# Performance work log

Hardware: AMD Instinct MI355X
Metric: run time of the kernel (lower is better)

## Reference

```python
import jax, jax.numpy as jnp
import numpy as np
from jax.scipy.special import logsumexp

B, T, D, H, K = 32, 512, 768, 256, 32


def setup_inputs() -> dict:
    key = jax.random.key(0)
    ks = jax.random.split(key, 12)
    x = jax.random.normal(ks[0], (B, T, D), jnp.float32)
    lengths = jax.random.randint(ks[1], (B,), T // 2, T + 1).astype(jnp.int32)
    mask = jnp.arange(T)[None, :] < lengths[:, None]  # [B,T] bool
    targets = jax.random.randint(ks[2], (B, T), 0, K)

    def p(k, shape, fan):
        return jax.random.normal(k, shape, jnp.float32) / np.sqrt(fan).astype(np.float32)

    W_ih_f = p(ks[3], (4 * H, D), D); W_hh_f = p(ks[4], (4 * H, H), H)
    W_ih_b = p(ks[5], (4 * H, D), D); W_hh_b = p(ks[6], (4 * H, H), H)
    b_f = jnp.zeros((4 * H,), jnp.float32); b_b = jnp.zeros((4 * H,), jnp.float32)
    W_clf = p(ks[7], (K, 2 * H), 2 * H); b_clf = jnp.zeros((K,), jnp.float32)
    start_t = jax.random.uniform(ks[8], (K,), jnp.float32, -0.1, 0.1)
    end_t = jax.random.uniform(ks[9], (K,), jnp.float32, -0.1, 0.1)
    trans = jax.random.uniform(ks[10], (K, K), jnp.float32, -0.1, 0.1)
    return {"input": x, "lengths": lengths, "mask": mask, "targets": targets,
            "W_ih_f": W_ih_f, "W_hh_f": W_hh_f, "b_f": b_f,
            "W_ih_b": W_ih_b, "W_hh_b": W_hh_b, "b_b": b_b,
            "W_clf": W_clf, "b_clf": b_clf,
            "start_t": start_t, "end_t": end_t, "trans": trans}


def _lstm_dir(x_tbd, W_ih, W_hh, b):
    # x_tbd: [T,B,D] -> hs [T,B,H], torch gate order (i,f,g,o)
    Hh = W_hh.shape[1]
    pre = jnp.einsum('tbd,gd->tbg', x_tbd, W_ih) + b  # precompute input projections

    def step(carry, p_t):
        h, c = carry
        g = p_t + h @ W_hh.T
        i, f, gg, o = jnp.split(g, 4, axis=-1)
        c = jax.nn.sigmoid(f) * c + jax.nn.sigmoid(i) * jnp.tanh(gg)
        h = jax.nn.sigmoid(o) * jnp.tanh(c)
        return (h, c), h

    b_sz = x_tbd.shape[1]
    init = (jnp.zeros((b_sz, Hh), x_tbd.dtype), jnp.zeros((b_sz, Hh), x_tbd.dtype))
    _, hs = jax.lax.scan(step, init, pre)
    return hs


def _emissions(x, lengths, W_ih_f, W_hh_f, b_f, W_ih_b, W_hh_b, b_b, W_clf, b_clf):
    Tn = x.shape[1]
    t_idx = jnp.arange(Tn)[None, :]
    # per-sequence reversal of the valid prefix (emulates packed bidirectional LSTM)
    rev_idx = jnp.where(t_idx < lengths[:, None], lengths[:, None] - 1 - t_idx, t_idx)
    h_f = _lstm_dir(x.transpose(1, 0, 2), W_ih_f, W_hh_f, b_f).transpose(1, 0, 2)
    x_rev = jnp.take_along_axis(x, rev_idx[:, :, None], axis=1)
    h_b = _lstm_dir(x_rev.transpose(1, 0, 2), W_ih_b, W_hh_b, b_b).transpose(1, 0, 2)
    h_b = jnp.take_along_axis(h_b, rev_idx[:, :, None], axis=1)  # un-flip
    hcat = jnp.concatenate([h_f, h_b], axis=-1)  # [B,T,2H]
    return hcat @ W_clf.T + b_clf  # [B,T,K]


def _crf_nll(em, targets, mask, lengths, start_t, end_t, trans):
    maskf = mask.astype(em.dtype)
    # numerator (gold path score)
    em_sc = jnp.take_along_axis(em, targets[:, :, None], axis=2)[..., 0]  # [B,T]
    tr_sc = trans[targets[:, :-1], targets[:, 1:]]  # [B,T-1]
    num = start_t[targets[:, 0]] + em_sc[:, 0] + jnp.sum((tr_sc + em_sc[:, 1:]) * maskf[:, 1:], axis=1)
    last_tags = jnp.take_along_axis(targets, (lengths - 1).astype(targets.dtype)[:, None], axis=1)[:, 0]
    num = num + end_t[last_tags]
    # log partition via forward algorithm
    def fwd_step(alpha, inp):
        e_t, m_t = inp
        nxt = logsumexp(alpha[:, :, None] + trans[None] + e_t[:, None, :], axis=1)
        return jnp.where(m_t[:, None], nxt, alpha), None

    alpha0 = start_t[None] + em[:, 0]
    alpha, _ = jax.lax.scan(fwd_step, alpha0, (em[:, 1:].transpose(1, 0, 2), mask[:, 1:].T))
    logZ = logsumexp(alpha + end_t[None], axis=1)
    return -jnp.mean(num - logZ)


def _viterbi(em, mask, start_t, end_t, trans):
    Kn = trans.shape[0]

    def vit_step(score, inp):
        e_t, m_t = inp
        bc = score[:, :, None] + trans[None] + e_t[:, None, :]  # [B,Kprev,Kcur]
        nxt = jnp.max(bc, axis=1)
        idx = jnp.argmax(bc, axis=1)  # [B,K] best previous tag
        idx = jnp.where(m_t[:, None], idx, jnp.arange(Kn)[None, :])  # identity on pads
        return jnp.where(m_t[:, None], nxt, score), idx

    score0 = start_t[None] + em[:, 0]
    score, hist = jax.lax.scan(vit_step, score0, (em[:, 1:].transpose(1, 0, 2), mask[:, 1:].T))
    last = jnp.argmax(score + end_t[None], axis=1)  # [B]

    def back(tag, h):
        prev = jnp.take_along_axis(h, tag[:, None], axis=1)[:, 0]
        return prev, prev

    _, tags_prev = jax.lax.scan(back, last, hist, reverse=True)  # [T-1,B]
    tags = jnp.concatenate([tags_prev, last[None]], axis=0).T  # [B,T]
    return jnp.where(mask, tags, 0)  # zero_pad


def reference(input, lengths, mask, targets, W_ih_f, W_hh_f, b_f, W_ih_b, W_hh_b, b_b,
              W_clf, b_clf, start_t, end_t, trans):
    em = _emissions(input, lengths, W_ih_f, W_hh_f, b_f, W_ih_b, W_hh_b, b_b, W_clf, b_clf)
    loss = _crf_nll(em, targets, mask, lengths, start_t, end_t, trans)
    preds = _viterbi(em, mask, start_t, end_t, trans)
    return loss, preds
```

## Files before the change

kernel.cpp:

```cpp
#include <hip/hip_runtime.h>
#include <hip/hip_bf16.h>


#define NB 32
#define NT 512
#define ND 768
#define NH 256
#define NK 32

__global__ __launch_bounds__(256) void k_sgemm(const float* __restrict__ A,
                                               const float* __restrict__ Wf,
                                               const float* __restrict__ Wb,
                                               float* __restrict__ C) {
    __shared__ float As[16][132];
    __shared__ float Bs[16][132];
    const int tid = threadIdx.x;
    const int bx = blockIdx.x;
    const int by = blockIdx.y;
    const int tx = tid & 15, ty = tid >> 4;
    const int sm = tid >> 2;
    const int sk = (tid & 3) * 4;
    float acc[8][8];
#pragma unroll
    for (int i = 0; i < 8; ++i)
#pragma unroll
        for (int j = 0; j < 8; ++j) acc[i][j] = 0.f;

    for (int k0 = 0; k0 < ND; k0 += 16) {
#pragma unroll
        for (int h = 0; h < 2; ++h) {
            int m = sm + h * 64;
            float4 v = *(const float4*)(A + (size_t)(by * 128 + m) * ND + k0 + sk);
            As[sk + 0][m] = v.x; As[sk + 1][m] = v.y; As[sk + 2][m] = v.z; As[sk + 3][m] = v.w;
            int n = sm + h * 64;
            int gn = bx * 128 + n;
            const float* Wrow = (gn < 1024) ? (Wf + (size_t)gn * ND) : (Wb + (size_t)(gn - 1024) * ND);
            float4 w = *(const float4*)(Wrow + k0 + sk);
            Bs[sk + 0][n] = w.x; Bs[sk + 1][n] = w.y; Bs[sk + 2][n] = w.z; Bs[sk + 3][n] = w.w;
        }
        __syncthreads();
#pragma unroll
        for (int kk = 0; kk < 16; ++kk) {
            float a[8], b[8];
            *(float4*)&a[0] = *(const float4*)&As[kk][ty * 4];
            *(float4*)&a[4] = *(const float4*)&As[kk][64 + ty * 4];
            *(float4*)&b[0] = *(const float4*)&Bs[kk][tx * 4];
            *(float4*)&b[4] = *(const float4*)&Bs[kk][64 + tx * 4];
#pragma unroll
            for (int i = 0; i < 8; ++i)
#pragma unroll
                for (int j = 0; j < 8; ++j)
                    acc[i][j] = fmaf(a[i], b[j], acc[i][j]);
        }
        __syncthreads();
    }
#pragma unroll
    for (int i = 0; i < 8; ++i) {
        int m = by * 128 + ((i < 4) ? (ty * 4 + i) : (64 + ty * 4 + (i - 4)));
        float* Crow = C + (size_t)m * 2048 + bx * 128;
        *(float4*)(Crow + tx * 4)      = make_float4(acc[i][0], acc[i][1], acc[i][2], acc[i][3]);
        *(float4*)(Crow + 64 + tx * 4) = make_float4(acc[i][4], acc[i][5], acc[i][6], acc[i][7]);
    }
}

__global__ __launch_bounds__(256) void k_wt4(const float* __restrict__ Whf,
                                             const float* __restrict__ Whb,
                                             float4* __restrict__ Wt4) {
    int gid = blockIdx.x * 256 + threadIdx.x;
    if (gid >= 131072) return;
    int dir = gid >> 16;
    int k   = (gid >> 8) & 255;
    int j   = gid & 255;
    const float* W = dir ? Whb : Whf;
    Wt4[gid] = make_float4(W[(size_t)(0 * 256 + j) * 256 + k],
                           W[(size_t)(1 * 256 + j) * 256 + k],
                           W[(size_t)(2 * 256 + j) * 256 + k],
                           W[(size_t)(3 * 256 + j) * 256 + k]);
}

__device__ __forceinline__ float sigm(float x) { return 1.f / (1.f + expf(-x)); }

__global__ __launch_bounds__(256, 1) void k_lstm3(const float* __restrict__ C,
                                                  const float4* __restrict__ Wt4,
                                                  const float* __restrict__ b_f,
                                                  const float* __restrict__ b_b,
                                                  const int* __restrict__ lengths,
                                                  float* __restrict__ h_f,
                                                  float* __restrict__ h_b) {
    __shared__ float4 hsh4[64];
    __shared__ float4 part[4][64];
    __shared__ float4 bias4[64];
    const int tid = threadIdx.x;
    const int g = blockIdx.x & 63, s = blockIdx.x >> 6;
    const int b = g & 31, dir = g >> 5;
    const int j0 = s * 64;
    const float* bias = dir ? b_b : b_f;
    float* hdir = dir ? h_b : h_f;

    if (tid < 64)
        bias4[tid] = make_float4(bias[j0 + tid], bias[256 + j0 + tid],
                                 bias[512 + j0 + tid], bias[768 + j0 + tid]);

    const int jj = tid & 63, kq = tid >> 6;
    float4 wreg[64];
    {
        const float4* wb = Wt4 + ((size_t)dir * 256 + kq * 64) * 256 + j0 + jj;
#pragma unroll
        for (int i = 0; i < 64; ++i) wreg[i] = wb[(size_t)i * 256];
    }
    const int mylen = lengths[b];
    float creg = 0.f;
    float* hshf = (float*)hsh4;
    __syncthreads();

    for (int t = 0; t < NT; ++t) {
        float4 pre = make_float4(0.f, 0.f, 0.f, 0.f);
        if (tid < 64) {
            int src_t = t;
            if (dir) src_t = (t < mylen) ? (mylen - 1 - t) : t;
            const float* Crow = C + (size_t)(b * 512 + src_t) * 2048 + dir * 1024 + j0 + tid;
            pre.x = Crow[0]; pre.y = Crow[256]; pre.z = Crow[512]; pre.w = Crow[768];
        }
        if (t > 0) {
            const float* hp = hdir + ((size_t)b * 512 + (t - 1)) * 256 + tid;
            float v;
            int guard = 0;
            for (;;) {
                v = __hip_atomic_load(hp, __ATOMIC_RELAXED, __HIP_MEMORY_SCOPE_AGENT);
                if (__float_as_uint(v) != 0xFFFFFFFFu) break;
                if (++guard > (1 << 22)) break;
            }
            hshf[tid] = v;
            __syncthreads();
        }
        float4 acc = make_float4(0.f, 0.f, 0.f, 0.f);
        if (t > 0) {
#pragma unroll
            for (int c = 0; c < 16; ++c) {
                float ha[4];
                *(float4*)ha = hsh4[kq * 16 + c];
#pragma unroll
                for (int i = 0; i < 4; ++i) {
                    float4 wv = wreg[c * 4 + i];
                    acc.x = fmaf(wv.x, ha[i], acc.x);
                    acc.y = fmaf(wv.y, ha[i], acc.y);
                    acc.z = fmaf(wv.z, ha[i], acc.z);
                    acc.w = fmaf(wv.w, ha[i], acc.w);
                }
            }
        }
        part[kq][jj] = acc;
        __syncthreads();
        if (tid < 64) {
            float4 b4 = bias4[tid];
            float sx = pre.x + b4.x, sy = pre.y + b4.y, sz = pre.z + b4.z, sw = pre.w + b4.w;
#pragma unroll
            for (int q = 0; q < 4; ++q) {
                float4 p = part[q][tid];
                sx += p.x; sy += p.y; sz += p.z; sw += p.w;
            }
            float ig = sigm(sx), fg = sigm(sy), gt = tanhf(sz), og = sigm(sw);
            creg = fg * creg + ig * gt;
            float hn = og * tanhf(creg);
            __hip_atomic_store(hdir + ((size_t)b * 512 + t) * 256 + j0 + tid,
                               hn, __ATOMIC_RELAXED, __HIP_MEMORY_SCOPE_AGENT);
        }
    }
}

__global__ __launch_bounds__(256) void k_em(const float* __restrict__ hf,
                                            const float* __restrict__ hb,
                                            const float* __restrict__ Wclf,
                                            const float* __restrict__ bclf,
                                            const int* __restrict__ lengths,
                                            float* __restrict__ em) {
    extern __shared__ float4 wc4[];
    const int tid = threadIdx.x;
    for (int idx = tid; idx < 4096; idx += 256) {
        int jq = idx >> 5, ko = idx & 31;
        wc4[idx] = *(const float4*)(Wclf + (size_t)ko * 512 + jq * 4);
    }
    __syncthreads();
    const int r = tid >> 5, ko = tid & 31;
    const int m = blockIdx.x * 8 + r;
    const int b = m >> 9, t = m & 511;
    const int len = lengths[b];
    const int rev = (t < len) ? (len - 1 - t) : t;
    const float* hfr = hf + (size_t)m * 256;
    const float* hbr = hb + (size_t)(b * 512 + rev) * 256;
    float acc = bclf[ko];
#pragma unroll 4
    for (int jq = 0; jq < 64; ++jq) {
        float4 h4 = *(const float4*)(hfr + jq * 4);
        float4 ww = wc4[jq * 32 + ko];
        acc += h4.x * ww.x + h4.y * ww.y + h4.z * ww.z + h4.w * ww.w;
    }
#pragma unroll 4
    for (int jq = 0; jq < 64; ++jq) {
        float4 h4 = *(const float4*)(hbr + jq * 4);
        float4 ww = wc4[(64 + jq) * 32 + ko];
        acc += h4.x * ww.x + h4.y * ww.y + h4.z * ww.z + h4.w * ww.w;
    }
    em[(size_t)m * 32 + ko] = acc;
}

__global__ __launch_bounds__(64) void k_crfvit(const float* __restrict__ em,
                                               const int* __restrict__ targets,
                                               const int* __restrict__ lengths,
                                               const float* __restrict__ start_t,
                                               const float* __restrict__ end_t,
                                               const float* __restrict__ trans,
                                               float* __restrict__ numv,
                                               float* __restrict__ logZv,
                                               float* __restrict__ out) {
    __shared__ float trans_s[32][33];
    __shared__ float vec[32];
    __shared__ unsigned char hist[511 * 32];
    const int tid = threadIdx.x;
    const int b = blockIdx.x & 31;
    const int mode = blockIdx.x >> 5;
    for (int idx = tid; idx < 1024; idx += 64) trans_s[idx >> 5][idx & 31] = trans[idx];
    const int len = lengths[b];
    const float* emb = em + (size_t)b * 512 * 32;
    const int k = tid & 31, half = tid >> 5;
    if (tid < 32) vec[tid] = start_t[tid] + emb[tid];
    __syncthreads();

    if (mode == 0) {
        for (int t = 1; t < NT; ++t) {
            bool mv = t < len;
            int kp0 = half * 16;
            float m = -1e30f;
#pragma unroll 4
            for (int i = 0; i < 16; ++i)
                m = fmaxf(m, vec[kp0 + i] + trans_s[kp0 + i][k]);
            float m2 = fmaxf(m, __shfl_xor(m, 32));
            float ssum = 0.f;
#pragma unroll 4
            for (int i = 0; i < 16; ++i)
                ssum += __expf(vec[kp0 + i] + trans_s[kp0 + i][k] - m2);
            ssum += __shfl_xor(ssum, 32);
            float anew = m2 + __logf(ssum) + emb[t * 32 + k];
            __syncthreads();
            if (half == 0 && mv) vec[k] = anew;
            __syncthreads();
        }
        float val = (tid < 32) ? vec[tid] + end_t[tid] : -1e30f;
        float m = val;
#pragma unroll
        for (int off = 32; off >= 1; off >>= 1) m = fmaxf(m, __shfl_xor(m, off));
        float e = (tid < 32) ? __expf(val - m) : 0.f;
#pragma unroll
        for (int off = 32; off >= 1; off >>= 1) e += __shfl_xor(e, off);
        if (tid == 0) logZv[b] = m + __logf(e);
        const int* tg = targets + b * 512;
        float partial = 0.f;
        for (int t = 1 + tid; t < NT; t += 64) {
            if (t < len) {
                int y0 = tg[t - 1], y1 = tg[t];
                partial += trans_s[y0][y1] + emb[t * 32 + y1];
            }
        }
#pragma unroll
        for (int off = 32; off >= 1; off >>= 1) partial += __shfl_xor(partial, off);
        if (tid == 0) {
            int y00 = tg[0];
            int yl = tg[len - 1];
            numv[b] = partial + start_t[y00] + emb[y00] + end_t[yl];
        }
    } else {
        for (int t = 1; t < NT; ++t) {
            bool mv = t < len;
            int kp0 = half * 16;
            float e = emb[t * 32 + k];
            float m = -1e30f; int mi = kp0;
#pragma unroll 4
            for (int i = 0; i < 16; ++i) {
                float v = (vec[kp0 + i] + trans_s[kp0 + i][k]) + e;
                if (v > m) { m = v; mi = kp0 + i; }
            }
            float mo = __shfl_xor(m, 32);
            int io = __shfl_xor(mi, 32);
            float mlow = half ? mo : m;   int ilow = half ? io : mi;
            float mhigh = half ? m : mo;  int ihigh = half ? mi : io;
            float bm; int bi;
            if (mhigh > mlow) { bm = mhigh; bi = ihigh; } else { bm = mlow; bi = ilow; }
            __syncthreads();
            if (half == 0) {
                hist[(t - 1) * 32 + k] = (unsigned char)(mv ? bi : k);
                if (mv) vec[k] = bm;
            }
            __syncthreads();
        }
        float val = (tid < 32) ? vec[tid] + end_t[tid] : -1e30f;
        int idx = (tid < 32) ? tid : 63;
#pragma unroll
        for (int off = 32; off >= 1; off >>= 1) {
            float vo = __shfl_xor(val, off);
            int io = __shfl_xor(idx, off);
            if (vo > val || (vo == val && io < idx)) { val = vo; idx = io; }
        }
        int cur = idx;
        float* ob = out + 1 + (size_t)b * 512;
        if (tid == 0) ob[511] = (511 < len) ? (float)cur : 0.f;
        for (int t2 = 510; t2 >= 0; --t2) {
            cur = hist[t2 * 32 + cur];
            if (tid == 0) ob[t2] = (t2 < len) ? (float)cur : 0.f;
        }
    }
}

__global__ __launch_bounds__(64) void k_loss(const float* __restrict__ numv,
                                             const float* __restrict__ logZv,
                                             float* __restrict__ out) {
    int tid = threadIdx.x;
    float v = (tid < 32) ? (logZv[tid] - numv[tid]) : 0.f;
#pragma unroll
    for (int off = 32; off >= 1; off >>= 1) v += __shfl_xor(v, off);
    if (tid == 0) out[0] = v / 32.f;
}

extern "C" void kernel_launch(void* const* d_in, const int* in_sizes, int n_in,
                              void* d_out, int out_size, void* d_ws, size_t ws_size,
                              hipStream_t stream) {
    const float* x       = (const float*)d_in[0];
    const int*   lengths = (const int*)d_in[1];
    const int*   targets = (const int*)d_in[3];
    const float* W_ih_f  = (const float*)d_in[4];
    const float* W_hh_f  = (const float*)d_in[5];
    const float* b_f     = (const float*)d_in[6];
    const float* W_ih_b  = (const float*)d_in[7];
    const float* W_hh_b  = (const float*)d_in[8];
    const float* b_b     = (const float*)d_in[9];
    const float* W_clf   = (const float*)d_in[10];
    const float* b_clf   = (const float*)d_in[11];
    const float* start_t = (const float*)d_in[12];
    const float* end_t   = (const float*)d_in[13];
    const float* trans   = (const float*)d_in[14];
    float* out = (float*)d_out;
    float* ws = (float*)d_ws;

    float* C     = ws;
    float* h_f   = C + (size_t)16384 * 2048;
    float* h_b   = h_f + (size_t)32 * 512 * 256;
    float* em    = h_b + (size_t)32 * 512 * 256;
    float4* Wt4  = (float4*)(em + (size_t)32 * 512 * 32);
    float* numv  = (float*)(Wt4 + 131072);
    float* logZv = numv + 32;

    hipMemsetAsync(h_f, 0xFF, (size_t)2 * 32 * 512 * 256 * sizeof(float), stream);
    k_wt4<<<512, 256, 0, stream>>>(W_hh_f, W_hh_b, Wt4);
    k_sgemm<<<dim3(16, 128), 256, 0, stream>>>(x, W_ih_f, W_ih_b, C);
    k_lstm3<<<256, 256, 0, stream>>>(C, Wt4, b_f, b_b, lengths, h_f, h_b);
    k_em<<<2048, 256, 65536, stream>>>(h_f, h_b, W_clf, b_clf, lengths, em);
    k_crfvit<<<64, 64, 0, stream>>>(em, targets, lengths, start_t, end_t, trans, numv, logZv, out);
    k_loss<<<1, 64, 0, stream>>>(numv, logZv, out);
}
```

Baseline: 2.477 ms.

## Fuse input-projection GEMM with LSTM recurrence using flag-based producer/consumer overlap

Merges the input-projection SGEMM and the recurrent LSTM kernel into one launch. GEMM blocks come first and are ordered by when the recurrence will need each row tile. LSTM blocks poll C for a 0xFF sentinel until their pre-activations arrive, so the recurrence can start before the whole GEMM is done. The cost is an extra 128 MB memset of C, atomic stores and loads, and spin-waiting. The scheme also relies on the GEMM blocks being scheduled ahead of the persistent LSTM blocks, or it could deadlock or starve.

```diff
diff --git a/kernel.cpp b/kernel.cpp
--- a/kernel.cpp
+++ b/kernel.cpp
@@ -7,61 +7,6 @@
 #define ND 768
 #define NH 256
 #define NK 32
-
-__global__ __launch_bounds__(256) void k_sgemm(const float* __restrict__ A,
-                                               const float* __restrict__ Wf,
-                                               const float* __restrict__ Wb,
-                                               float* __restrict__ C) {
-    __shared__ float As[16][132];
-    __shared__ float Bs[16][132];
-    const int tid = threadIdx.x;
-    const int bx = blockIdx.x;
-    const int by = blockIdx.y;
-    const int tx = tid & 15, ty = tid >> 4;
-    const int sm = tid >> 2;
-    const int sk = (tid & 3) * 4;
-    float acc[8][8];
-#pragma unroll
-    for (int i = 0; i < 8; ++i)
-#pragma unroll
-        for (int j = 0; j < 8; ++j) acc[i][j] = 0.f;
-
-    for (int k0 = 0; k0 < ND; k0 += 16) {
-#pragma unroll
-        for (int h = 0; h < 2; ++h) {
-            int m = sm + h * 64;
-            float4 v = *(const float4*)(A + (size_t)(by * 128 + m) * ND + k0 + sk);
-            As[sk + 0][m] = v.x; As[sk + 1][m] = v.y; As[sk + 2][m] = v.z; As[sk + 3][m] = v.w;
-            int n = sm + h * 64;
-            int gn = bx * 128 + n;
-            const float* Wrow = (gn < 1024) ? (Wf + (size_t)gn * ND) : (Wb + (size_t)(gn - 1024) * ND);
-            float4 w = *(const float4*)(Wrow + k0 + sk);
-            Bs[sk + 0][n] = w.x; Bs[sk + 1][n] = w.y; Bs[sk + 2][n] = w.z; Bs[sk + 3][n] = w.w;
-        }
-        __syncthreads();
-#pragma unroll
-        for (int kk = 0; kk < 16; ++kk) {
-            float a[8], b[8];
-            *(float4*)&a[0] = *(const float4*)&As[kk][ty * 4];
-            *(float4*)&a[4] = *(const float4*)&As[kk][64 + ty * 4];
-            *(float4*)&b[0] = *(const float4*)&Bs[kk][tx * 4];
-            *(float4*)&b[4] = *(const float4*)&Bs[kk][64 + tx * 4];
-#pragma unroll
-            for (int i = 0; i < 8; ++i)
-#pragma unroll
-                for (int j = 0; j < 8; ++j)
-                    acc[i][j] = fmaf(a[i], b[j], acc[i][j]);
-        }
-        __syncthreads();
-    }
-#pragma unroll
-    for (int i = 0; i < 8; ++i) {
-        int m = by * 128 + ((i < 4) ? (ty * 4 + i) : (64 + ty * 4 + (i - 4)));
-        float* Crow = C + (size_t)m * 2048 + bx * 128;
-        *(float4*)(Crow + tx * 4)      = make_float4(acc[i][0], acc[i][1], acc[i][2], acc[i][3]);
-        *(float4*)(Crow + 64 + tx * 4) = make_float4(acc[i][4], acc[i][5], acc[i][6], acc[i][7]);
-    }
-}
 
 __global__ __launch_bounds__(256) void k_wt4(const float* __restrict__ Whf,
                                              const float* __restrict__ Whb,
@@ -80,18 +25,110 @@
 
 __device__ __forceinline__ float sigm(float x) { return 1.f / (1.f + expf(-x)); }
 
-__global__ __launch_bounds__(256, 1) void k_lstm3(const float* __restrict__ C,
+__global__ __launch_bounds__(256, 1) void k_fused(const float* __restrict__ A,
+                                                  const float* __restrict__ Wf,
+                                                  const float* __restrict__ Wb,
+                                                  float* __restrict__ C,
                                                   const float4* __restrict__ Wt4,
                                                   const float* __restrict__ b_f,
                                                   const float* __restrict__ b_b,
                                                   const int* __restrict__ lengths,
                                                   float* __restrict__ h_f,
                                                   float* __restrict__ h_b) {
+    __shared__ float As[16][132];
+    __shared__ float Bs[16][132];
+    __shared__ int keys[128];
+    __shared__ int sched[128];
     __shared__ float4 hsh4[64];
     __shared__ float4 part[4][64];
     __shared__ float4 bias4[64];
+
     const int tid = threadIdx.x;
-    const int g = blockIdx.x & 63, s = blockIdx.x >> 6;
+    const int bid = blockIdx.x;
+
+    if (bid < 2048) {
+        if (tid < 128) {
+            int b = tid >> 2, q = tid & 3;
+            int len = lengths[b];
+            int lo = q * 128, hi = lo + 127;
+            int fwd = lo;
+            int bwd;
+            if (len - 1 > hi)       bwd = len - 1 - hi;
+            else if (len - 1 >= lo) bwd = 0;
+            else                    bwd = lo;
+            int need = fwd < bwd ? fwd : bwd;
+            keys[tid] = need * 128 + tid;
+        }
+        __syncthreads();
+        if (tid < 128) {
+            int my = keys[tid];
+            int rank = 0;
+#pragma unroll 4
+            for (int y = 0; y < 128; ++y) rank += (keys[y] < my);
+            sched[rank] = tid;
+        }
+        __syncthreads();
+
+        const int by = sched[bid >> 4];
+        const int bx = bid & 15;
+        const int tx = tid & 15, ty = tid >> 4;
+        const int sm = tid >> 2;
+        const int sk = (tid & 3) * 4;
+        float acc[8][8];
+#pragma unroll
+        for (int i = 0; i < 8; ++i)
+#pragma unroll
+            for (int j = 0; j < 8; ++j) acc[i][j] = 0.f;
+
+        for (int k0 = 0; k0 < ND; k0 += 16) {
+#pragma unroll
+            for (int h = 0; h < 2; ++h) {
+                int m = sm + h * 64;
+                float4 v = *(const float4*)(A + (size_t)(by * 128 + m) * ND + k0 + sk);
+                As[sk + 0][m] = v.x; As[sk + 1][m] = v.y; As[sk + 2][m] = v.z; As[sk + 3][m] = v.w;
+                int n = sm + h * 64;
+                int gn = bx * 128 + n;
+                const float* Wrow = (gn < 1024) ? (Wf + (size_t)gn * ND) : (Wb + (size_t)(gn - 1024) * ND);
+                float4 w = *(const float4*)(Wrow + k0 + sk);
+                Bs[sk + 0][n] = w.x; Bs[sk + 1][n] = w.y; Bs[sk + 2][n] = w.z; Bs[sk + 3][n] = w.w;
+            }
+            __syncthreads();
+#pragma unroll
+            for (int kk = 0; kk < 16; ++kk) {
+                float a[8], b[8];
+                *(float4*)&a[0] = *(const float4*)&As[kk][ty * 4];
+                *(float4*)&a[4] = *(const float4*)&As[kk][64 + ty * 4];
+                *(float4*)&b[0] = *(const float4*)&Bs[kk][tx * 4];
+                *(float4*)&b[4] = *(const float4*)&Bs[kk][64 + tx * 4];
+#pragma unroll
+                for (int i = 0; i < 8; ++i)
+#pragma unroll
+                    for (int j = 0; j < 8; ++j)
+                        acc[i][j] = fmaf(a[i], b[j], acc[i][j]);
+            }
+            __syncthreads();
+        }
+#pragma unroll
+        for (int i = 0; i < 8; ++i) {
+            int m = by * 128 + ((i < 4) ? (ty * 4 + i) : (64 + ty * 4 + (i - 4)));
+            float* Crow = C + (size_t)m * 2048 + bx * 128;
+#pragma unroll
+            for (int hh = 0; hh < 2; ++hh) {
+                float* p = Crow + hh * 64 + tx * 4;
+#pragma unroll
+                for (int w = 0; w < 2; ++w) {
+                    float2 v = make_float2(acc[i][hh * 4 + 2 * w], acc[i][hh * 4 + 2 * w + 1]);
+                    __hip_atomic_store((unsigned long long*)(p + 2 * w),
+                                       *(unsigned long long*)&v,
+                                       __ATOMIC_RELAXED, __HIP_MEMORY_SCOPE_AGENT);
+                }
+            }
+        }
+        return;
+    }
+
+    const int lid = bid - 2048;
+    const int g = lid & 63, s = lid >> 6;
     const int b = g & 31, dir = g >> 5;
     const int j0 = s * 64;
     const float* bias = dir ? b_b : b_f;
@@ -115,11 +152,15 @@
 
     for (int t = 0; t < NT; ++t) {
         float4 pre = make_float4(0.f, 0.f, 0.f, 0.f);
+        const float* Crow = nullptr;
         if (tid < 64) {
             int src_t = t;
             if (dir) src_t = (t < mylen) ? (mylen - 1 - t) : t;
-            const float* Crow = C + (size_t)(b * 512 + src_t) * 2048 + dir * 1024 + j0 + tid;
-            pre.x = Crow[0]; pre.y = Crow[256]; pre.z = Crow[512]; pre.w = Crow[768];
+            Crow = C + (size_t)(b * 512 + src_t) * 2048 + dir * 1024 + j0 + tid;
+            pre.x = __hip_atomic_load(Crow + 0,   __ATOMIC_RELAXED, __HIP_MEMORY_SCOPE_AGENT);
+            pre.y = __hip_atomic_load(Crow + 256, __ATOMIC_RELAXED, __HIP_MEMORY_SCOPE_AGENT);
+            pre.z = __hip_atomic_load(Crow + 512, __ATOMIC_RELAXED, __HIP_MEMORY_SCOPE_AGENT);
+            pre.w = __hip_atomic_load(Crow + 768, __ATOMIC_RELAXED, __HIP_MEMORY_SCOPE_AGENT);
         }
         if (t > 0) {
             const float* hp = hdir + ((size_t)b * 512 + (t - 1)) * 256 + tid;
@@ -152,6 +193,20 @@
         part[kq][jj] = acc;
         __syncthreads();
         if (tid < 64) {
+            {
+                int guard = 0;
+                while (__float_as_uint(pre.x) == 0xFFFFFFFFu ||
+                       __float_as_uint(pre.y) == 0xFFFFFFFFu ||
+                       __float_as_uint(pre.z) == 0xFFFFFFFFu ||
+                       __float_as_uint(pre.w) == 0xFFFFFFFFu) {
+                    __builtin_amdgcn_s_sleep(2);
+                    pre.x = __hip_atomic_load(Crow + 0,   __ATOMIC_RELAXED, __HIP_MEMORY_SCOPE_AGENT);
+                    pre.y = __hip_atomic_load(Crow + 256, __ATOMIC_RELAXED, __HIP_MEMORY_SCOPE_AGENT);
+                    pre.z = __hip_atomic_load(Crow + 512, __ATOMIC_RELAXED, __HIP_MEMORY_SCOPE_AGENT);
+                    pre.w = __hip_atomic_load(Crow + 768, __ATOMIC_RELAXED, __HIP_MEMORY_SCOPE_AGENT);
+                    if (++guard > (1 << 22)) break;
+                }
+            }
             float4 b4 = bias4[tid];
             float sx = pre.x + b4.x, sy = pre.y + b4.y, sz = pre.z + b4.z, sw = pre.w + b4.w;
 #pragma unroll
@@ -348,10 +403,11 @@
     float* numv  = (float*)(Wt4 + 131072);
     float* logZv = numv + 32;
 
+    hipMemsetAsync(C,   0xFF, (size_t)16384 * 2048 * sizeof(float), stream);
     hipMemsetAsync(h_f, 0xFF, (size_t)2 * 32 * 512 * 256 * sizeof(float), stream);
     k_wt4<<<512, 256, 0, stream>>>(W_hh_f, W_hh_b, Wt4);
-    k_sgemm<<<dim3(16, 128), 256, 0, stream>>>(x, W_ih_f, W_ih_b, C);
-    k_lstm3<<<256, 256, 0, stream>>>(C, Wt4, b_f, b_b, lengths, h_f, h_b);
+    k_fused<<<2304, 256, 0, stream>>>(x, W_ih_f, W_ih_b, C, Wt4, b_f, b_b,
+                                      lengths, h_f, h_b);
     k_em<<<2048, 256, 65536, stream>>>(h_f, h_b, W_clf, b_clf, lengths, em);
     k_crfvit<<<64, 64, 0, stream>>>(em, targets, lengths, start_t, end_t, trans, numv, logZv, out);
     k_loss<<<1, 64, 0, stream>>>(numv, logZv, out);
```

After: 2.790 ms. 1.13x slower.

## Remove block barriers from LSTM recurrence and double-buffer SGEMM shared tiles

Applied to the files above, without the earlier changes.

The LSTM step kernel is restructured so each wave polls the full previous hidden vector itself with 64-bit atomic loads. It stages that vector into a per-wave shared buffer and reduces the four k-partials with cross-lane shuffles instead of a shared partial array. This removes both __syncthreads per timestep on the serial critical path. The input-projection SGEMM is also double-buffered, prefetching the next k tile into registers while computing the current one, which halves the barriers per iteration. The costs are four times the polling traffic per block, and correctness that relies on wave-local LDS ordering enforced by an explicit waitcnt and sched_barrier.

```diff
diff --git a/kernel.cpp b/kernel.cpp
--- a/kernel.cpp
+++ b/kernel.cpp
@@ -12,8 +12,8 @@
                                                const float* __restrict__ Wf,
                                                const float* __restrict__ Wb,
                                                float* __restrict__ C) {
-    __shared__ float As[16][132];
-    __shared__ float Bs[16][132];
+    __shared__ float As[2][16][132];
+    __shared__ float Bs[2][16][132];
     const int tid = threadIdx.x;
     const int bx = blockIdx.x;
     const int by = blockIdx.y;
@@ -26,33 +26,56 @@
 #pragma unroll
         for (int j = 0; j < 8; ++j) acc[i][j] = 0.f;
 
+    const float* Arow0 = A + (size_t)(by * 128 + sm) * ND + sk;
+    const float* Arow1 = A + (size_t)(by * 128 + 64 + sm) * ND + sk;
+    const int gn0 = bx * 128 + sm, gn1 = gn0 + 64;
+    const float* W0 = (gn0 < 1024) ? (Wf + (size_t)gn0 * ND + sk) : (Wb + (size_t)(gn0 - 1024) * ND + sk);
+    const float* W1 = (gn1 < 1024) ? (Wf + (size_t)gn1 * ND + sk) : (Wb + (size_t)(gn1 - 1024) * ND + sk);
+
+    {
+        float4 a0 = *(const float4*)(Arow0);
+        float4 a1 = *(const float4*)(Arow1);
+        float4 w0 = *(const float4*)(W0);
+        float4 w1 = *(const float4*)(W1);
+        As[0][sk + 0][sm] = a0.x; As[0][sk + 1][sm] = a0.y; As[0][sk + 2][sm] = a0.z; As[0][sk + 3][sm] = a0.w;
+        As[0][sk + 0][64 + sm] = a1.x; As[0][sk + 1][64 + sm] = a1.y; As[0][sk + 2][64 + sm] = a1.z; As[0][sk + 3][64 + sm] = a1.w;
+        Bs[0][sk + 0][sm] = w0.x; Bs[0][sk + 1][sm] = w0.y; Bs[0][sk + 2][sm] = w0.z; Bs[0][sk + 3][sm] = w0.w;
+        Bs[0][sk + 0][64 + sm] = w1.x; Bs[0][sk + 1][64 + sm] = w1.y; Bs[0][sk + 2][64 + sm] = w1.z; Bs[0][sk + 3][64 + sm] = w1.w;
+    }
+    __syncthreads();
+
+    int cur = 0;
     for (int k0 = 0; k0 < ND; k0 += 16) {
-#pragma unroll
-        for (int h = 0; h < 2; ++h) {
-            int m = sm + h * 64;
-            float4 v = *(const float4*)(A + (size_t)(by * 128 + m) * ND + k0 + sk);
-            As[sk + 0][m] = v.x; As[sk + 1][m] = v.y; As[sk + 2][m] = v.z; As[sk + 3][m] = v.w;
-            int n = sm + h * 64;
-            int gn = bx * 128 + n;
-            const float* Wrow = (gn < 1024) ? (Wf + (size_t)gn * ND) : (Wb + (size_t)(gn - 1024) * ND);
-            float4 w = *(const float4*)(Wrow + k0 + sk);
-            Bs[sk + 0][n] = w.x; Bs[sk + 1][n] = w.y; Bs[sk + 2][n] = w.z; Bs[sk + 3][n] = w.w;
-        }
-        __syncthreads();
+        const bool more = (k0 + 16) < ND;
+        float4 na0, na1, nw0, nw1;
+        if (more) {
+            na0 = *(const float4*)(Arow0 + k0 + 16);
+            na1 = *(const float4*)(Arow1 + k0 + 16);
+            nw0 = *(const float4*)(W0 + k0 + 16);
+            nw1 = *(const float4*)(W1 + k0 + 16);
+        }
 #pragma unroll
         for (int kk = 0; kk < 16; ++kk) {
             float a[8], b[8];
-            *(float4*)&a[0] = *(const float4*)&As[kk][ty * 4];
-            *(float4*)&a[4] = *(const float4*)&As[kk][64 + ty * 4];
-            *(float4*)&b[0] = *(const float4*)&Bs[kk][tx * 4];
-            *(float4*)&b[4] = *(const float4*)&Bs[kk][64 + tx * 4];
+            *(float4*)&a[0] = *(const float4*)&As[cur][kk][ty * 4];
+            *(float4*)&a[4] = *(const float4*)&As[cur][kk][64 + ty * 4];
+            *(float4*)&b[0] = *(const float4*)&Bs[cur][kk][tx * 4];
+            *(float4*)&b[4] = *(const float4*)&Bs[cur][kk][64 + tx * 4];
 #pragma unroll
             for (int i = 0; i < 8; ++i)
 #pragma unroll
                 for (int j = 0; j < 8; ++j)
                     acc[i][j] = fmaf(a[i], b[j], acc[i][j]);
         }
-        __syncthreads();
+        if (more) {
+            const int nxt = cur ^ 1;
+            As[nxt][sk + 0][sm] = na0.x; As[nxt][sk + 1][sm] = na0.y; As[nxt][sk + 2][sm] = na0.z; As[nxt][sk + 3][sm] = na0.w;
+            As[nxt][sk + 0][64 + sm] = na1.x; As[nxt][sk + 1][64 + sm] = na1.y; As[nxt][sk + 2][64 + sm] = na1.z; As[nxt][sk + 3][64 + sm] = na1.w;
+            Bs[nxt][sk + 0][sm] = nw0.x; Bs[nxt][sk + 1][sm] = nw0.y; Bs[nxt][sk + 2][sm] = nw0.z; Bs[nxt][sk + 3][sm] = nw0.w;
+            Bs[nxt][sk + 0][64 + sm] = nw1.x; Bs[nxt][sk + 1][64 + sm] = nw1.y; Bs[nxt][sk + 2][64 + sm] = nw1.z; Bs[nxt][sk + 3][64 + sm] = nw1.w;
+            __syncthreads();
+            cur = nxt;
+        }
     }
 #pragma unroll
     for (int i = 0; i < 8; ++i) {
@@ -80,16 +103,14 @@
 
 __device__ __forceinline__ float sigm(float x) { return 1.f / (1.f + expf(-x)); }
 
-__global__ __launch_bounds__(256, 1) void k_lstm3(const float* __restrict__ C,
+__global__ __launch_bounds__(256, 1) void k_lstm4(const float* __restrict__ C,
                                                   const float4* __restrict__ Wt4,
                                                   const float* __restrict__ b_f,
                                                   const float* __restrict__ b_b,
                                                   const int* __restrict__ lengths,
                                                   float* __restrict__ h_f,
                                                   float* __restrict__ h_b) {
-    __shared__ float4 hsh4[64];
-    __shared__ float4 part[4][64];
-    __shared__ float4 bias4[64];
+    __shared__ float hsh[4][272];
     const int tid = threadIdx.x;
     const int g = blockIdx.x & 63, s = blockIdx.x >> 6;
     const int b = g & 31, dir = g >> 5;
@@ -97,48 +118,62 @@
     const float* bias = dir ? b_b : b_f;
     float* hdir = dir ? h_b : h_f;
 
-    if (tid < 64)
-        bias4[tid] = make_float4(bias[j0 + tid], bias[256 + j0 + tid],
-                                 bias[512 + j0 + tid], bias[768 + j0 + tid]);
-
-    const int jj = tid & 63, kq = tid >> 6;
+    const int j = tid >> 2;
+    const int kq = tid & 3;
+    const int w = tid >> 6;
+    const int lane = tid & 63;
+
     float4 wreg[64];
     {
-        const float4* wb = Wt4 + ((size_t)dir * 256 + kq * 64) * 256 + j0 + jj;
+        const float4* wb = Wt4 + ((size_t)dir * 256 + kq * 64) * 256 + j0 + j;
 #pragma unroll
         for (int i = 0; i < 64; ++i) wreg[i] = wb[(size_t)i * 256];
     }
+    float4 breg = make_float4(0.f, 0.f, 0.f, 0.f);
+    if (kq == 0)
+        breg = make_float4(bias[j0 + j], bias[256 + j0 + j],
+                           bias[512 + j0 + j], bias[768 + j0 + j]);
     const int mylen = lengths[b];
     float creg = 0.f;
-    float* hshf = (float*)hsh4;
-    __syncthreads();
 
     for (int t = 0; t < NT; ++t) {
         float4 pre = make_float4(0.f, 0.f, 0.f, 0.f);
-        if (tid < 64) {
+        if (kq == 0) {
             int src_t = t;
             if (dir) src_t = (t < mylen) ? (mylen - 1 - t) : t;
-            const float* Crow = C + (size_t)(b * 512 + src_t) * 2048 + dir * 1024 + j0 + tid;
+            const float* Crow = C + (size_t)(b * 512 + src_t) * 2048 + dir * 1024 + j0 + j;
             pre.x = Crow[0]; pre.y = Crow[256]; pre.z = Crow[512]; pre.w = Crow[768];
         }
+        float4 acc = make_float4(0.f, 0.f, 0.f, 0.f);
         if (t > 0) {
-            const float* hp = hdir + ((size_t)b * 512 + (t - 1)) * 256 + tid;
-            float v;
+            const float* hp = hdir + ((size_t)b * 512 + (t - 1)) * 256 + 4 * lane;
+            unsigned long long u0, u1;
             int guard = 0;
             for (;;) {
-                v = __hip_atomic_load(hp, __ATOMIC_RELAXED, __HIP_MEMORY_SCOPE_AGENT);
-                if (__float_as_uint(v) != 0xFFFFFFFFu) break;
-                if (++guard > (1 << 22)) break;
-            }
-            hshf[tid] = v;
-            __syncthreads();
-        }
-        float4 acc = make_float4(0.f, 0.f, 0.f, 0.f);
-        if (t > 0) {
+                u0 = __hip_atomic_load((const unsigned long long*)hp,
+                                       __ATOMIC_RELAXED, __HIP_MEMORY_SCOPE_AGENT);
+                u1 = __hip_atomic_load((const unsigned long long*)(hp + 2),
+                                       __ATOMIC_RELAXED, __HIP_MEMORY_SCOPE_AGENT);
+                if ((unsigned)(u0 & 0xFFFFFFFFu) != 0xFFFFFFFFu &&
+                    (unsigned)(u0 >> 32)        != 0xFFFFFFFFu &&
+                    (unsigned)(u1 & 0xFFFFFFFFu) != 0xFFFFFFFFu &&
+                    (unsigned)(u1 >> 32)        != 0xFFFFFFFFu) break;
+                if (++guard > (1 << 24)) break;
+            }
+            const int d0 = 4 * lane;
+            float* dst = &hsh[w][(d0 >> 6) * 68 + (d0 & 63)];
+            float lo0 = __uint_as_float((unsigned)(u0 & 0xFFFFFFFFu));
+            float hi0 = __uint_as_float((unsigned)(u0 >> 32));
+            float lo1 = __uint_as_float((unsigned)(u1 & 0xFFFFFFFFu));
+            float hi1 = __uint_as_float((unsigned)(u1 >> 32));
+            *(float4*)dst = make_float4(lo0, hi0, lo1, hi1);
+            asm volatile("s_waitcnt lgkmcnt(0)" ::: "memory");
+            __builtin_amdgcn_sched_barrier(0);
+            const float* src = &hsh[w][kq * 68];
 #pragma unroll
             for (int c = 0; c < 16; ++c) {
                 float ha[4];
-                *(float4*)ha = hsh4[kq * 16 + c];
+                *(float4*)ha = *(const float4*)(src + 4 * c);
 #pragma unroll
                 for (int i = 0; i < 4; ++i) {
                     float4 wv = wreg[c * 4 + i];
@@ -149,22 +184,23 @@
                 }
             }
         }
-        part[kq][jj] = acc;
-        __syncthreads();
-        if (tid < 64) {
-            float4 b4 = bias4[tid];
-            float sx = pre.x + b4.x, sy = pre.y + b4.y, sz = pre.z + b4.z, sw = pre.w + b4.w;
-#pragma unroll
-            for (int q = 0; q < 4; ++q) {
-                float4 p = part[q][tid];
-                sx += p.x; sy += p.y; sz += p.z; sw += p.w;
-            }
-            float ig = sigm(sx), fg = sigm(sy), gt = tanhf(sz), og = sigm(sw);
-            creg = fg * creg + ig * gt;
-            float hn = og * tanhf(creg);
-            __hip_atomic_store(hdir + ((size_t)b * 512 + t) * 256 + j0 + tid,
-                               hn, __ATOMIC_RELAXED, __HIP_MEMORY_SCOPE_AGENT);
-        }
+        if (kq == 0) {
+            acc.x += pre.x + breg.x; acc.y += pre.y + breg.y;
+            acc.z += pre.z + breg.z; acc.w += pre.w + breg.w;
+        }
+#pragma unroll
+        for (int off = 1; off <= 2; off <<= 1) {
+            acc.x += __shfl_xor(acc.x, off);
+            acc.y += __shfl_xor(acc.y, off);
+            acc.z += __shfl_xor(acc.z, off);
+            acc.w += __shfl_xor(acc.w, off);
+        }
+        float ig = sigm(acc.x), fg = sigm(acc.y), gt = tanhf(acc.z), og = sigm(acc.w);
+        creg = fg * creg + ig * gt;
+        float hn = og * tanhf(creg);
+        if (kq == 0)
+            __hip_atomic_store(hdir + ((size_t)b * 512 + t) * 256 + j0 + j, hn,
+                               __ATOMIC_RELAXED, __HIP_MEMORY_SCOPE_AGENT);
     }
 }
 
@@ -351,7 +387,7 @@
     hipMemsetAsync(h_f, 0xFF, (size_t)2 * 32 * 512 * 256 * sizeof(float), stream);
     k_wt4<<<512, 256, 0, stream>>>(W_hh_f, W_hh_b, Wt4);
     k_sgemm<<<dim3(16, 128), 256, 0, stream>>>(x, W_ih_f, W_ih_b, C);
-    k_lstm3<<<256, 256, 0, stream>>>(C, Wt4, b_f, b_b, lengths, h_f, h_b);
+    k_lstm4<<<256, 256, 0, stream>>>(C, Wt4, b_f, b_b, lengths, h_f, h_b);
     k_em<<<2048, 256, 65536, stream>>>(h_f, h_b, W_clf, b_clf, lengths, em);
     k_crfvit<<<64, 64, 0, stream>>>(em, targets, lengths, start_t, end_t, trans, numv, logZv, out);
     k_loss<<<1, 64, 0, stream>>>(numv, logZv, out);
```

Measured after the change: 2.563 ms. 1.03x slower.
